# Optimization experiments

Hardware: AMD Instinct MI355X
Metric: run time of the kernel (lower is better)

## Reference

```python
import jax, jax.numpy as jnp
import numpy as np
from jax import lax

S = 224          # raster_settings.image_size
K = 10           # raster_settings.faces_per_pixel
BLUR = 1e-4      # raster_settings.blur_radius (signed squared-dist threshold)
SIGMA = 1e-4     # BlendParams().sigma used by sigmoid_alpha_blend
BIG = 1e10
AREA_EPS = 1e-10


def setup_inputs():
    key = jax.random.key(0)
    k1, k2, k3 = jax.random.split(key, 3)
    B, V, F = 2, 5023, 5000
    xy = jax.random.uniform(k1, (B, V, 2), minval=-1.0, maxval=1.0)
    z = jax.random.uniform(k2, (B, V, 1), minval=0.5, maxval=1.5)
    vertices = jnp.concatenate([xy, z], -1).astype(jnp.float32)
    faces = jax.random.randint(k3, (B, F, 3), 0, V, dtype=jnp.int32)
    return {"vertices": vertices, "faces": faces}


def _cross2(a, b):
    return a[..., 0] * b[..., 1] - a[..., 1] * b[..., 0]


def _edge_d2(a, b, p):
    # squared distance from points p [W,1,2] to segment (a,b) [F,2] -> [W,F]
    ab = b - a
    ap = p - a
    t = jnp.clip((ap * ab).sum(-1) / jnp.maximum((ab * ab).sum(-1), 1e-12), 0.0, 1.0)
    proj = a + t[..., None] * ab
    return ((p - proj) ** 2).sum(-1)


def _rasterize_one(verts, faces):
    # naive PyTorch3D-style rasterizer for one mesh: per pixel, keep K nearest
    # faces (by interpolated z) whose signed squared dist to the triangle < BLUR.
    tri = verts[faces]                                  # [F,3,3]
    v0, v1, v2 = tri[:, 0, :2], tri[:, 1, :2], tri[:, 2, :2]
    z0, z1, z2 = tri[:, 0, 2], tri[:, 1, 2], tri[:, 2, 2]
    area = _cross2(v1 - v0, v2 - v0)
    good_face = jnp.abs(area) > AREA_EPS                # cull degenerate faces
    area_safe = jnp.where(good_face, area, 1.0)
    # NDC pixel centers (pytorch3d convention: +x left, +y up; verts pre-negated)
    coords = 1.0 - (2.0 * jnp.arange(S, dtype=verts.dtype) + 1.0) / S

    def row(yf):
        p = jnp.stack([coords, jnp.full((S,), yf, verts.dtype)], -1)[:, None, :]  # [W,1,2]
        w0 = _cross2(v2 - v1, p - v1) / area_safe       # [W,F] barycentric
        w1 = _cross2(v0 - v2, p - v2) / area_safe
        w2 = _cross2(v1 - v0, p - v0) / area_safe
        z = w0 * z0 + w1 * z1 + w2 * z2                  # no perspective correction (default)
        inside = (w0 > 0) & (w1 > 0) & (w2 > 0)
        d2 = jnp.minimum(jnp.minimum(_edge_d2(v0, v1, p), _edge_d2(v1, v2, p)),
                         _edge_d2(v2, v0, p))
        sd = jnp.where(inside, -d2, d2)                  # signed squared dist
        valid = good_face & (z > 0) & (sd <= BLUR)
        negz = jnp.where(valid, -z, -BIG)
        vals, idx = lax.top_k(negz, K)                   # K nearest by z
        vk = vals > -0.5 * BIG
        zk = jnp.take_along_axis(z, idx, -1)
        dk = jnp.take_along_axis(sd, idx, -1)
        return (jnp.where(vk, idx, -1), jnp.where(vk, zk, -1.0), jnp.where(vk, dk, -1.0))

    return lax.map(row, coords)                          # each [S,S,K]


def reference(vertices, faces):
    B, V, _ = vertices.shape
    F = faces.shape[1]
    fixed = vertices * jnp.array([-1.0, -1.0, 1.0], vertices.dtype)  # flip x,y (DECA)
    p2f_l, zbuf, dists = jax.vmap(_rasterize_one)(fixed, faces)      # [B,S,S,K]
    mask = p2f_l >= 0
    # packed (global) pix_to_face like pytorch3d
    p2f = jnp.where(mask, p2f_l + (jnp.arange(B) * F)[:, None, None, None], -1)
    # sigmoid_alpha_blend: alpha = 1 - prod(1 - sigmoid(-dist/sigma))
    prob = jax.nn.sigmoid(-dists / SIGMA) * mask
    alpha = 1.0 - jnp.prod(1.0 - prob, -1)               # [B,S,S]
    images = alpha[:, None, :, :]                        # images[...,3:].permute(0,3,1,2)
    # vertex visibility from nearest face per pixel (scatter)
    faces_packed = (faces + V * jnp.arange(B, dtype=faces.dtype)[:, None, None]).reshape(-1, 3)
    faces_all = jnp.concatenate([faces_packed, -jnp.ones((1, 3), faces.dtype)], 0)
    vis_verts = faces_all[p2f[..., 0].reshape(-1)].reshape(-1)  # -1 wraps to sentinel row
    vv = jnp.zeros(B * V + 1, vertices.dtype).at[vis_verts].set(1.0)
    visibility = vv[:-1].reshape(B, V)                   # extra slot absorbs -1 indices
    return images, visibility
```

## Files before the change

### kernel.cpp

```cpp
#include <hip/hip_runtime.h>
#include <math.h>

#define SDIM 224
#define KTOP 10
#define NB 2
#define NV 5023
#define NF 5000
#define BLUR 1e-4f
#define IMG_SZ (NB * SDIM * SDIM)
#define NW 8
#define SEG (NF / NW)
#define CAP 1024
#define HT 0.031251f
#define COV_THR 0.04422f
#define REL_THR (-0.0543f)

__device__ __forceinline__ float seg_d2_exact(float ax, float ay, float abx, float aby,
                                              float L, float px, float py) {
    float apx = __fsub_rn(px, ax), apy = __fsub_rn(py, ay);
    float dot = __fadd_rn(__fmul_rn(apx, abx), __fmul_rn(apy, aby));
    float t = __fdiv_rn(dot, L);
    t = fminf(fmaxf(t, 0.0f), 1.0f);
    float prx = __fadd_rn(ax, __fmul_rn(t, abx));
    float pry = __fadd_rn(ay, __fmul_rn(t, aby));
    float dx = __fsub_rn(px, prx), dy = __fsub_rn(py, pry);
    return __fadd_rn(__fmul_rn(dx, dx), __fmul_rn(dy, dy));
}

__global__ void preprocess_kernel(const float* __restrict__ verts,
                                  const int* __restrict__ faces,
                                  float4* __restrict__ ga,
                                  float4* __restrict__ hh,
                                  float4* __restrict__ cc,
                                  float* __restrict__ out)
{
    const int idx = blockIdx.x * blockDim.x + threadIdx.x;
    if (idx < NB * NV) out[IMG_SZ + idx] = 0.0f;
    if (idx >= NB * NF) return;
    const int b = idx / NF;
    const int* fp = faces + (size_t)idx * 3;
    const int i0 = fp[0], i1 = fp[1], i2 = fp[2];
    const float* vb = verts + (size_t)b * NV * 3;
    const float v0x = -vb[i0*3+0], v0y = -vb[i0*3+1], z0 = vb[i0*3+2];
    const float v1x = -vb[i1*3+0], v1y = -vb[i1*3+1], z1 = vb[i1*3+2];
    const float v2x = -vb[i2*3+0], v2y = -vb[i2*3+1], z2 = vb[i2*3+2];
    const float e01x = __fsub_rn(v1x, v0x), e01y = __fsub_rn(v1y, v0y);
    const float e12x = __fsub_rn(v2x, v1x), e12y = __fsub_rn(v2y, v1y);
    const float e20x = __fsub_rn(v0x, v2x), e20y = __fsub_rn(v0y, v2y);
    const float area = __fsub_rn(__fmul_rn(e01x, __fsub_rn(v2y, v0y)),
                                 __fmul_rn(e01y, __fsub_rn(v2x, v0x)));
    const bool good = fabsf(area) > 1e-10f;
    const float area_safe = good ? area : 1.0f;

    double Zx = 0.0, Zy = 0.0, Zc = 0.0;
    float mgc = -1.0f;
    float n0x=0,n0y=0,n0c=-3e38f, n1x=0,n1y=0,n1c=-3e38f, n2x=0,n2y=0,n2c=-3e38f;
    if (good) {
        const double invA = 1.0 / (double)area;
        const double c0c = (double)e12y*v1x - (double)e12x*v1y;
        const double c1c = (double)e20y*v2x - (double)e20x*v2y;
        const double c2c = (double)e01y*v0x - (double)e01x*v0y;
        Zx = (-(double)e12y*z0 - (double)e20y*z1 - (double)e01y*z2) * invA;
        Zy = ( (double)e12x*z0 + (double)e20x*z1 + (double)e01x*z2) * invA;
        Zc = (c0c*z0 + c1c*z1 + c2c*z2) * invA;
        const double B0 = fabs((double)e12x)*(1.0+fabs((double)v1y)) + fabs((double)e12y)*(1.0+fabs((double)v1x));
        const double B1 = fabs((double)e20x)*(1.0+fabs((double)v2y)) + fabs((double)e20y)*(1.0+fabs((double)v2x));
        const double B2 = fabs((double)e01x)*(1.0+fabs((double)v0y)) + fabs((double)e01y)*(1.0+fabs((double)v0x));
        const double B = (B0*(double)z0 + B1*(double)z1 + B2*(double)z2) * fabs(invA);
        mgc = (float)(2.5e-6 * B) + 1e-20f;
        const double s = (area > 0.0f) ? 1.0 : -1.0;
        const double l12 = sqrt((double)e12x*e12x + (double)e12y*e12y);
        const double l20 = sqrt((double)e20x*e20x + (double)e20y*e20y);
        const double l01 = sqrt((double)e01x*e01x + (double)e01y*e01y);
        const double i12 = s / fmax(l12, 1e-300);
        const double i20 = s / fmax(l20, 1e-300);
        const double i01 = s / fmax(l01, 1e-300);
        n0x = (float)(-(double)e12y * i12);
        n0y = (float)( (double)e12x * i12);
        n0c = (float)(((double)e12y*v1x - (double)e12x*v1y) * i12);
        n1x = (float)(-(double)e20y * i20);
        n1y = (float)( (double)e20x * i20);
        n1c = (float)(((double)e20y*v2x - (double)e20x*v2y) * i20);
        n2x = (float)(-(double)e01y * i01);
        n2y = (float)( (double)e01x * i01);
        n2c = (float)(((double)e01y*v0x - (double)e01x*v0y) * i01);
    }
    ga[idx]     = make_float4((float)Zx, (float)Zy, (float)Zc, mgc);
    cc[3*idx+0] = make_float4(n0x, n0y, n0c, n1x);
    cc[3*idx+1] = make_float4(n1y, n1c, n2x, n2y);
    cc[3*idx+2] = make_float4(n2c, 0.0f, 0.0f, 0.0f);
    hh[3*idx+0] = make_float4(v0x, v0y, v1x, v1y);
    hh[3*idx+1] = make_float4(v2x, v2y, z0, z1);
    hh[3*idx+2] = make_float4(z2, area_safe, 0.0f, 0.0f);
}

__device__ __forceinline__ void heavy_face(float4 h0, float4 h1, float4 h2,
                                           int fidx, bool pass, float px, float py,
                                           float tz[KTOP], float ts[KTOP],
                                           float& bestZ, int& bestIdx)
{
    if (!pass) return;
    const float v0x=h0.x, v0y=h0.y, v1x=h0.z, v1y=h0.w;
    const float v2x=h1.x, v2y=h1.y, z0=h1.z, z1=h1.w;
    const float z2=h2.x, area=h2.y;
    const float e01x = __fsub_rn(v1x, v0x), e01y = __fsub_rn(v1y, v0y);
    const float e12x = __fsub_rn(v2x, v1x), e12y = __fsub_rn(v2y, v1y);
    const float e20x = __fsub_rn(v0x, v2x), e20y = __fsub_rn(v0y, v2y);

    const float c0 = __fsub_rn(__fmul_rn(e12x, __fsub_rn(py, v1y)),
                               __fmul_rn(e12y, __fsub_rn(px, v1x)));
    const float c1 = __fsub_rn(__fmul_rn(e20x, __fsub_rn(py, v2y)),
                               __fmul_rn(e20y, __fsub_rn(px, v2x)));
    const float c2 = __fsub_rn(__fmul_rn(e01x, __fsub_rn(py, v0y)),
                               __fmul_rn(e01y, __fsub_rn(px, v0x)));

    const float L01 = fmaxf(__fadd_rn(__fmul_rn(e01x,e01x), __fmul_rn(e01y,e01y)), 1e-12f);
    const float L12 = fmaxf(__fadd_rn(__fmul_rn(e12x,e12x), __fmul_rn(e12y,e12y)), 1e-12f);
    const float L20 = fmaxf(__fadd_rn(__fmul_rn(e20x,e20x), __fmul_rn(e20y,e20y)), 1e-12f);

    const bool ap = area > 0.0f;
    const bool s0 = ap ? (c0 > 0.0f) : (c0 < 0.0f);
    const bool s1 = ap ? (c1 > 0.0f) : (c1 < 0.0f);
    const bool s2 = ap ? (c2 > 0.0f) : (c2 < 0.0f);
    if (!(s0 & s1 & s2)) {
        bool cull = false;
        if (!s0) cull |= (c0 * c0 > BLUR * 1.0002f * L12);
        if (!s1) cull |= (c1 * c1 > BLUR * 1.0002f * L20);
        if (!s2) cull |= (c2 * c2 > BLUR * 1.0002f * L01);
        if (cull) return;
    }

    const float w0 = __fdiv_rn(c0, area);
    const float w1 = __fdiv_rn(c1, area);
    const float w2 = __fdiv_rn(c2, area);
    const float z = __fadd_rn(__fadd_rn(__fmul_rn(w0, z0), __fmul_rn(w1, z1)),
                              __fmul_rn(w2, z2));
    if (!(z > 0.0f)) return;
    if (!(z < tz[KTOP-1])) return;

    const bool inside = (w0 > 0.0f) & (w1 > 0.0f) & (w2 > 0.0f);
    float sd;
    if (inside) {
        const bool sat = (c0*c0 >= 1.0002e-3f * L12) &
                         (c1*c1 >= 1.0002e-3f * L20) &
                         (c2*c2 >= 1.0002e-3f * L01);
        if (sat) {
            sd = -1.0f;
        } else {
            const float d2 = fminf(fminf(
                seg_d2_exact(v0x, v0y, e01x, e01y, L01, px, py),
                seg_d2_exact(v1x, v1y, e12x, e12y, L12, px, py)),
                seg_d2_exact(v2x, v2y, e20x, e20y, L20, px, py));
            sd = -d2;
        }
    } else {
        const float d2 = fminf(fminf(
            seg_d2_exact(v0x, v0y, e01x, e01y, L01, px, py),
            seg_d2_exact(v1x, v1y, e12x, e12y, L12, px, py)),
            seg_d2_exact(v2x, v2y, e20x, e20y, L20, px, py));
        if (!(d2 <= BLUR)) return;
        sd = d2;
    }

    if (z < bestZ) { bestZ = z; bestIdx = fidx; }

    float cz = z, cs = sd;
#pragma unroll
    for (int j = 0; j < KTOP; ++j) {
        if (cz < tz[j]) {
            const float oz = tz[j], os = ts[j];
            tz[j] = cz; ts[j] = cs; cz = oz; cs = os;
        }
    }
}

__global__ __launch_bounds__(64 * NW, 6) void raster_kernel(const float4* __restrict__ gaG,
                                                            const float4* __restrict__ hhG,
                                                            const float4* __restrict__ ccG,
                                                            const int* __restrict__ faces,
                                                            float* __restrict__ out)
{
    const int b = blockIdx.z;
    const int lane = threadIdx.x & 63;
    const int w = __builtin_amdgcn_readfirstlane((int)(threadIdx.x >> 6));
    const int x = (blockIdx.x << 3) + (lane & 7);
    const int y = (blockIdx.y << 3) + (lane >> 3);
    const float px = __fsub_rn(1.0f, __fdiv_rn(__fadd_rn(__fmul_rn(2.0f, (float)x), 1.0f), (float)SDIM));
    const float py = __fsub_rn(1.0f, __fdiv_rn(__fadd_rn(__fmul_rn(2.0f, (float)y), 1.0f), (float)SDIM));
    const float pcx = __fsub_rn(1.0f, __fdiv_rn((float)(16 * blockIdx.x + 8), 224.0f));
    const float pcy = __fsub_rn(1.0f, __fdiv_rn((float)(16 * blockIdx.y + 8), 224.0f));

    __shared__ int   sList[CAP];
    __shared__ int   sHist[64];
    __shared__ int   sCnt[NW];
    __shared__ int   sOff[NW];
    __shared__ int   sLen;
    __shared__ float sT;
    __shared__ float sZ[NW][64][11];
    __shared__ float sS[NW][64][11];
    __shared__ float sBZ[NW][64];
    __shared__ int   sBI[NW][64];

    if (threadIdx.x < 64) sHist[threadIdx.x] = 0;
    __syncthreads();

    const float4* __restrict__ ga = gaG + (size_t)b * NF;
    const float4* __restrict__ hh = hhG + (size_t)b * NF * 3;
    const float4* __restrict__ cc = ccG + (size_t)b * NF * 3;

    const int f0 = w * SEG, f1 = f0 + SEG;
    float dm[10], zl[10], zh[10];
#pragma unroll
    for (int it = 0; it < 10; ++it) {
        const int f = f0 + it * 64 + lane;
        dm[it] = -3e38f; zl[it] = 3e38f; zh[it] = -3e38f;
        if (f < f1) {
            const float4 a0 = ga[f];
            const float4 cA = cc[3*f+0];
            const float4 cB = cc[3*f+1];
            const float4 cC = cc[3*f+2];
            const float d0 = fmaf(cA.x, pcx, fmaf(cA.y, pcy, cA.z));
            const float d1 = fmaf(cA.w, pcx, fmaf(cB.x, pcy, cB.y));
            const float d2 = fmaf(cB.z, pcx, fmaf(cB.w, pcy, cC.x));
            const float dmin = fminf(d0, fminf(d1, d2));
            const float ztc = fmaf(a0.x, pcx, fmaf(a0.y, pcy, a0.z));
            const float spread = fmaf(fabsf(a0.x), HT, fmaf(fabsf(a0.y), HT, 2.0f * fabsf(a0.w))) + 1e-6f;
            dm[it] = dmin; zl[it] = ztc - spread; zh[it] = ztc + spread;
            if ((a0.w > 0.0f) && (dmin >= COV_THR) && (zl[it] > 0.0f)) {
                int bk = (int)floorf((zh[it] - 0.4f) * 53.333332f);
                bk = max(0, min(63, bk));
                atomicAdd(&sHist[bk], 1);
            }
        }
    }
    __syncthreads();

    if (threadIdx.x == 0) {
        int cum = 0; float T = 3e38f;
        for (int k2 = 0; k2 < 64; ++k2) {
            cum += sHist[k2];
            if (cum >= KTOP) { T = (k2 >= 63) ? 3e38f : (0.4f + (float)(k2+1) * 0.01875f + 1e-4f); break; }
        }
        sT = T;
    }
    __syncthreads();
    const float Tt = sT;

    int svMask = 0, cnt = 0;
#pragma unroll
    for (int it = 0; it < 10; ++it) {
        const bool sv = (dm[it] >= REL_THR) && (zl[it] <= Tt) && (zh[it] > 0.0f);
        if (sv) svMask |= (1 << it);
        cnt += (int)__popcll(__ballot(sv));
    }
    if (lane == 0) sCnt[w] = cnt;
    __syncthreads();
    if (threadIdx.x == 0) {
        int acc = 0;
        for (int w2 = 0; w2 < NW; ++w2) { sOff[w2] = acc; acc += sCnt[w2]; }
        sLen = (acc <= CAP) ? acc : -1;
    }
    __syncthreads();
    const int Ltot = sLen;

    if (Ltot >= 0) {
        const unsigned long long below = ((lane == 63) ? ~0ull : ((1ull << (lane + 1)) - 1ull)) >> 1;
        int woff = sOff[w];
#pragma unroll
        for (int it = 0; it < 10; ++it) {
            const bool sv = (svMask >> it) & 1;
            const unsigned long long m = __ballot(sv);
            if (sv) sList[woff + (int)__popcll(m & below)] = f0 + it * 64 + lane;
            woff += (int)__popcll(m);
        }
    }
    __syncthreads();

    float tz[KTOP], ts[KTOP];
#pragma unroll
    for (int j = 0; j < KTOP; ++j) { tz[j] = 3e38f; ts[j] = 3e38f; }
    float bestZ = 3e38f;
    int bestIdx = -1;

    if (Ltot >= 0) {
        const int chunk = (Ltot + NW - 1) / NW;
        const int jb = w * chunk, je = min(Ltot, jb + chunk);
        if (jb < je) {
            int fA = __builtin_amdgcn_readfirstlane(sList[jb]);
            int fB = __builtin_amdgcn_readfirstlane(sList[min(jb + 1, je - 1)]);
            float4 gC  = ga[fA];
            float4 hC0 = hh[3*fA+0], hC1 = hh[3*fA+1], hC2 = hh[3*fA+2];
            for (int j = jb; j < je; ++j) {
                const int fN = __builtin_amdgcn_readfirstlane(sList[min(j + 2, je - 1)]);
                const float4 gN  = ga[fB];
                const float4 hN0 = hh[3*fB+0], hN1 = hh[3*fB+1], hN2 = hh[3*fB+2];
                const float zt  = fmaf(gC.x, px, fmaf(gC.y, py, gC.z));
                const float thr = tz[KTOP-1];
                const bool pass = (zt > -gC.w) & (zt < thr + gC.w);
                if (__any(pass)) {
                    heavy_face(hC0, hC1, hC2, fA, pass, px, py, tz, ts, bestZ, bestIdx);
                }
                fA = fB; fB = fN;
                gC = gN; hC0 = hN0; hC1 = hN1; hC2 = hN2;
            }
        }
    } else {
        for (int f = f0; f < f1; ++f) {
            const float4 g = ga[f];
            const float zt  = fmaf(g.x, px, fmaf(g.y, py, g.z));
            const float thr = tz[KTOP-1];
            const bool pass = (zt > -g.w) & (zt < thr + g.w);
            if (__any(pass)) {
                heavy_face(hh[3*f+0], hh[3*f+1], hh[3*f+2], f, pass, px, py,
                           tz, ts, bestZ, bestIdx);
            }
        }
    }

#pragma unroll
    for (int j = 0; j < KTOP; ++j) { sZ[w][lane][j] = tz[j]; sS[w][lane][j] = ts[j]; }
    sZ[w][lane][KTOP] = 3e38f;
    sBZ[w][lane] = bestZ;
    sBI[w][lane] = bestIdx;
    __syncthreads();

    if (threadIdx.x < 64) {
        const int p = threadIdx.x;
        float bz = sBZ[0][p]; int bi = sBI[0][p];
#pragma unroll
        for (int w2 = 1; w2 < NW; ++w2) {
            if (sBZ[w2][p] < bz) { bz = sBZ[w2][p]; bi = sBI[w2][p]; }
        }
        int ptr[NW];
#pragma unroll
        for (int w2 = 0; w2 < NW; ++w2) ptr[w2] = 0;
        float prod = 1.0f;
#pragma unroll
        for (int k = 0; k < KTOP; ++k) {
            float mz = 3e38f; int mw = -1;
#pragma unroll
            for (int w2 = 0; w2 < NW; ++w2) {
                const float zc = sZ[w2][p][ptr[w2]];
                if (zc < mz) { mz = zc; mw = w2; }
            }
            float sd = 3e38f;
#pragma unroll
            for (int w2 = 0; w2 < NW; ++w2) {
                if (w2 == mw) { sd = sS[w2][p][ptr[w2]]; ptr[w2]++; }
            }
            prod *= 1.0f / (1.0f + __expf(-sd * 1e4f));
        }
        const float alpha = 1.0f - prod;
        const int gx = (blockIdx.x << 3) + (p & 7);
        const int gy = (blockIdx.y << 3) + (p >> 3);
        out[(size_t)b * (SDIM * SDIM) + gy * SDIM + gx] = alpha;

        if (bi >= 0) {
            const int* fp = faces + ((size_t)b * NF + bi) * 3;
            float* vis = out + IMG_SZ;
            vis[b * NV + fp[0]] = 1.0f;
            vis[b * NV + fp[1]] = 1.0f;
            vis[b * NV + fp[2]] = 1.0f;
        }
    }
}

extern "C" void kernel_launch(void* const* d_in, const int* in_sizes, int n_in,
                              void* d_out, int out_size, void* d_ws, size_t ws_size,
                              hipStream_t stream)
{
    const float* verts = (const float*)d_in[0];
    const int*   faces = (const int*)d_in[1];
    float* out = (float*)d_out;
    float4* ga = (float4*)d_ws;
    float4* hh = (float4*)((char*)d_ws + NB * NF * 16);
    float4* cc = (float4*)((char*)d_ws + NB * NF * (16 + 48));

    const int total = NB * NV;
    preprocess_kernel<<<dim3((total + 255) / 256), dim3(256), 0, stream>>>(verts, faces, ga, hh, cc, out);
    raster_kernel<<<dim3(SDIM / 8, SDIM / 8, NB), dim3(64 * NW), 0, stream>>>(ga, hh, cc, faces, out);
}
```

Baseline: 191.7 us.

## Add per-face z-range bounds to tighten candidate culling and raise list capacity

Preprocessing now computes per-face conservative min/max depth bounds, stored in spare slots of the cc buffer. The raster kernel's histogram threshold and candidate selection use these bounds to discard more faces. The per-pixel depth threshold is clamped by the tile threshold Tt, and the list capacity is raised so the compacted path is used more often. It also drops the software prefetch pipeline in the list loop, removes the separate bestZ shared buffer in favour of reading the top-k head, and relaxes the occupancy hint in launch bounds, which may raise register use and lose the overlap the prefetch provided.

```diff
diff --git a/kernel.cpp b/kernel.cpp
--- a/kernel.cpp
+++ b/kernel.cpp
@@ -10,7 +10,7 @@
 #define IMG_SZ (NB * SDIM * SDIM)
 #define NW 8
 #define SEG (NF / NW)
-#define CAP 1024
+#define CAP 1536
 #define HT 0.031251f
 #define COV_THR 0.04422f
 #define REL_THR (-0.0543f)
@@ -55,6 +55,7 @@
     double Zx = 0.0, Zy = 0.0, Zc = 0.0;
     float mgc = -1.0f;
     float n0x=0,n0y=0,n0c=-3e38f, n1x=0,n1y=0,n1c=-3e38f, n2x=0,n2y=0,n2c=-3e38f;
+    float zloF = 3e38f, zhiF = -1.0f;
     if (good) {
         const double invA = 1.0 / (double)area;
         const double c0c = (double)e12y*v1x - (double)e12x*v1y;
@@ -84,11 +85,17 @@
         n2x = (float)(-(double)e01y * i01);
         n2y = (float)( (double)e01x * i01);
         n2c = (float)(((double)e01y*v0x - (double)e01x*v0y) * i01);
+        const double gradZ = sqrt(Zx*Zx + Zy*Zy);
+        const double zminV = fmin((double)z0, fmin((double)z1, (double)z2));
+        const double zmaxV = fmax((double)z0, fmax((double)z1, (double)z2));
+        zloF = (float)(zminV - 0.0102 * gradZ - (double)mgc - 1e-6);
+        const bool elig = (zminV - (double)mgc - 1e-6) > 0.0;
+        zhiF = elig ? (float)(zmaxV + (double)mgc + 1e-6) : -1.0f;
     }
     ga[idx]     = make_float4((float)Zx, (float)Zy, (float)Zc, mgc);
     cc[3*idx+0] = make_float4(n0x, n0y, n0c, n1x);
     cc[3*idx+1] = make_float4(n1y, n1c, n2x, n2y);
-    cc[3*idx+2] = make_float4(n2c, 0.0f, 0.0f, 0.0f);
+    cc[3*idx+2] = make_float4(n2c, zloF, zhiF, 0.0f);
     hh[3*idx+0] = make_float4(v0x, v0y, v1x, v1y);
     hh[3*idx+1] = make_float4(v2x, v2y, z0, z1);
     hh[3*idx+2] = make_float4(z2, area_safe, 0.0f, 0.0f);
@@ -174,11 +181,11 @@
     }
 }
 
-__global__ __launch_bounds__(64 * NW, 6) void raster_kernel(const float4* __restrict__ gaG,
-                                                            const float4* __restrict__ hhG,
-                                                            const float4* __restrict__ ccG,
-                                                            const int* __restrict__ faces,
-                                                            float* __restrict__ out)
+__global__ __launch_bounds__(64 * NW) void raster_kernel(const float4* __restrict__ gaG,
+                                                         const float4* __restrict__ hhG,
+                                                         const float4* __restrict__ ccG,
+                                                         const int* __restrict__ faces,
+                                                         float* __restrict__ out)
 {
     const int b = blockIdx.z;
     const int lane = threadIdx.x & 63;
@@ -198,7 +205,6 @@
     __shared__ float sT;
     __shared__ float sZ[NW][64][11];
     __shared__ float sS[NW][64][11];
-    __shared__ float sBZ[NW][64];
     __shared__ int   sBI[NW][64];
 
     if (threadIdx.x < 64) sHist[threadIdx.x] = 0;
@@ -209,11 +215,11 @@
     const float4* __restrict__ cc = ccG + (size_t)b * NF * 3;
 
     const int f0 = w * SEG, f1 = f0 + SEG;
-    float dm[10], zl[10], zh[10];
+    float dm[10], zl[10];
 #pragma unroll
     for (int it = 0; it < 10; ++it) {
         const int f = f0 + it * 64 + lane;
-        dm[it] = -3e38f; zl[it] = 3e38f; zh[it] = -3e38f;
+        dm[it] = -3e38f; zl[it] = 3e38f;
         if (f < f1) {
             const float4 a0 = ga[f];
             const float4 cA = cc[3*f+0];
@@ -225,9 +231,11 @@
             const float dmin = fminf(d0, fminf(d1, d2));
             const float ztc = fmaf(a0.x, pcx, fmaf(a0.y, pcy, a0.z));
             const float spread = fmaf(fabsf(a0.x), HT, fmaf(fabsf(a0.y), HT, 2.0f * fabsf(a0.w))) + 1e-6f;
-            dm[it] = dmin; zl[it] = ztc - spread; zh[it] = ztc + spread;
-            if ((a0.w > 0.0f) && (dmin >= COV_THR) && (zl[it] > 0.0f)) {
-                int bk = (int)floorf((zh[it] - 0.4f) * 53.333332f);
+            dm[it] = dmin;
+            zl[it] = fmaxf(ztc - spread, cC.y);
+            if ((cC.z > 0.0f) && (dmin >= COV_THR)) {
+                const float zh = fminf(ztc + spread, cC.z);
+                int bk = (int)floorf((zh - 0.4f) * 53.333332f);
                 bk = max(0, min(63, bk));
                 atomicAdd(&sHist[bk], 1);
             }
@@ -249,7 +257,7 @@
     int svMask = 0, cnt = 0;
 #pragma unroll
     for (int it = 0; it < 10; ++it) {
-        const bool sv = (dm[it] >= REL_THR) && (zl[it] <= Tt) && (zh[it] > 0.0f);
+        const bool sv = (dm[it] >= REL_THR) && (zl[it] <= Tt);
         if (sv) svMask |= (1 << it);
         cnt += (int)__popcll(__ballot(sv));
     }
@@ -285,30 +293,22 @@
     if (Ltot >= 0) {
         const int chunk = (Ltot + NW - 1) / NW;
         const int jb = w * chunk, je = min(Ltot, jb + chunk);
-        if (jb < je) {
-            int fA = __builtin_amdgcn_readfirstlane(sList[jb]);
-            int fB = __builtin_amdgcn_readfirstlane(sList[min(jb + 1, je - 1)]);
-            float4 gC  = ga[fA];
-            float4 hC0 = hh[3*fA+0], hC1 = hh[3*fA+1], hC2 = hh[3*fA+2];
-            for (int j = jb; j < je; ++j) {
-                const int fN = __builtin_amdgcn_readfirstlane(sList[min(j + 2, je - 1)]);
-                const float4 gN  = ga[fB];
-                const float4 hN0 = hh[3*fB+0], hN1 = hh[3*fB+1], hN2 = hh[3*fB+2];
-                const float zt  = fmaf(gC.x, px, fmaf(gC.y, py, gC.z));
-                const float thr = tz[KTOP-1];
-                const bool pass = (zt > -gC.w) & (zt < thr + gC.w);
-                if (__any(pass)) {
-                    heavy_face(hC0, hC1, hC2, fA, pass, px, py, tz, ts, bestZ, bestIdx);
-                }
-                fA = fB; fB = fN;
-                gC = gN; hC0 = hN0; hC1 = hN1; hC2 = hN2;
+        for (int j = jb; j < je; ++j) {
+            const int f = __builtin_amdgcn_readfirstlane(sList[j]);
+            const float4 g = ga[f];
+            const float zt  = fmaf(g.x, px, fmaf(g.y, py, g.z));
+            const float thr = fminf(tz[KTOP-1], Tt);
+            const bool pass = (zt > -g.w) & (zt < thr + g.w);
+            if (__any(pass)) {
+                heavy_face(hh[3*f+0], hh[3*f+1], hh[3*f+2], f, pass, px, py,
+                           tz, ts, bestZ, bestIdx);
             }
         }
     } else {
         for (int f = f0; f < f1; ++f) {
             const float4 g = ga[f];
             const float zt  = fmaf(g.x, px, fmaf(g.y, py, g.z));
-            const float thr = tz[KTOP-1];
+            const float thr = fminf(tz[KTOP-1], Tt);
             const bool pass = (zt > -g.w) & (zt < thr + g.w);
             if (__any(pass)) {
                 heavy_face(hh[3*f+0], hh[3*f+1], hh[3*f+2], f, pass, px, py,
@@ -320,16 +320,16 @@
 #pragma unroll
     for (int j = 0; j < KTOP; ++j) { sZ[w][lane][j] = tz[j]; sS[w][lane][j] = ts[j]; }
     sZ[w][lane][KTOP] = 3e38f;
-    sBZ[w][lane] = bestZ;
     sBI[w][lane] = bestIdx;
     __syncthreads();
 
     if (threadIdx.x < 64) {
         const int p = threadIdx.x;
-        float bz = sBZ[0][p]; int bi = sBI[0][p];
+        float bz = sZ[0][p][0]; int bi = sBI[0][p];
 #pragma unroll
         for (int w2 = 1; w2 < NW; ++w2) {
-            if (sBZ[w2][p] < bz) { bz = sBZ[w2][p]; bi = sBI[w2][p]; }
+            const float zc = sZ[w2][p][0];
+            if (zc < bz) { bz = zc; bi = sBI[w2][p]; }
         }
         int ptr[NW];
 #pragma unroll
```

Result: faster. 187.5 us (-2.2%).
